# Kernel tuning notes

Measured on AMD Instinct MI355X. Metric: run time of the kernel, lower is better.

The kernel has to match this reference:

```python
import jax, jax.numpy as jnp
import numpy as np

B, N, D = 2, 2048, 2048
H, HKV, HD = 16, 4, 128  # n_heads, n_kv_heads, head_dim
G = H // HKV             # GQA group size


def setup_inputs() -> dict:
    key = jax.random.key(0)
    ks = jax.random.split(key, 5)
    x = jax.random.normal(ks[0], (B, N, D), jnp.float32)
    # rotary angles: standard 10000-base frequencies, half head_dim
    inv_freq = 1.0 / (10000.0 ** (jnp.arange(HD // 2, dtype=jnp.float32) / (HD // 2)))
    ang = jnp.arange(N, dtype=jnp.float32)[:, None] * inv_freq[None, :]  # [N, HD/2]
    cos = jnp.cos(ang)[None, :, None, :]  # [1, N, 1, HD/2]
    sin = jnp.sin(ang)[None, :, None, :]
    attn_mask = jnp.ones((B, N), jnp.float32)
    s = 0.02
    Wq = jax.random.normal(ks[1], (D, H * HD), jnp.float32) * s
    Wkv = jax.random.normal(ks[2], (D, 2 * HKV * HD), jnp.float32) * s
    Wo = jax.random.normal(ks[3], (H * HD, D), jnp.float32) * s
    bo = jnp.zeros((D,), jnp.float32)
    return {"x": x, "cos": cos, "sin": sin, "attn_mask": attn_mask,
            "Wq": Wq, "Wkv": Wkv, "Wo": Wo, "bo": bo}


def _rope(t, cos, sin):
    # t: [b, n, h, d]; rotate-half style split at d//2
    d2 = t.shape[-1] // 2
    t1, t2 = t[..., :d2], t[..., d2:]
    return jnp.concatenate([t1 * cos + t2 * sin, t2 * cos - t1 * sin], axis=-1)


def reference(x, cos, sin, attn_mask, Wq, Wkv, Wo, bo):
    b, n, _ = x.shape
    q = (x @ Wq).reshape(b, n, H, HD)
    kv = x @ Wkv
    k, v = jnp.split(kv, 2, axis=-1)
    k = k.reshape(b, n, HKV, HD)
    v = v.reshape(b, n, HKV, HD)
    q = _rope(q, cos, sin)
    k = _rope(k, cos, sin)
    # b n h d -> b h n d; group q heads: head H_idx maps to kv head H_idx % HKV
    # (einops '(r h)' repeat pattern => q reshaped as [b, G, HKV, n, d])
    q = q.transpose(0, 2, 1, 3).reshape(b, G, HKV, n, HD)
    k = k.transpose(0, 2, 1, 3)  # [b, HKV, n, d]
    v = v.transpose(0, 2, 1, 3)
    scale = HD ** -0.5
    attn = jnp.einsum('bghnd,bhmd->bghnm', q, k) * scale
    bias = (1.0 - attn_mask) * -1e9  # [b, n_keys]
    attn = attn + bias[:, None, None, None, :]
    attn = jax.nn.softmax(attn, axis=-1)
    out = jnp.einsum('bghnm,bhmd->bghnd', attn, v)
    # b (g h) n d -> b n (g h d)
    out = out.transpose(0, 3, 1, 2, 4).reshape(b, n, H * HD)
    return out @ Wo + bo
```

## Files before the change

### kernel.cpp

```cpp
#include <hip/hip_runtime.h>
#include <hip/hip_bf16.h>
#include <cstddef>

#define NB    2
#define NSEQ  2048
#define DMODEL 2048
#define NH    16
#define NKV   4
#define HDIM  128

typedef __attribute__((ext_vector_type(8))) short short8;
typedef __attribute__((ext_vector_type(4))) short short4v;
typedef __attribute__((ext_vector_type(4))) float floatx4;
typedef const __attribute__((address_space(1))) void* gptr_t;
typedef __attribute__((address_space(3))) void* lptr_t;

#if __has_builtin(__builtin_amdgcn_exp2f)
#define EXP2F(x) __builtin_amdgcn_exp2f(x)
#else
#define EXP2F(x) __expf((x) * 0.6931471805599453f)
#endif

__device__ inline unsigned short f2bf(float f) {
    unsigned int u = __float_as_uint(f);
    u += 0x7fffu + ((u >> 16) & 1u);
    return (unsigned short)(u >> 16);
}

__device__ inline unsigned int pk2bf_trunc(float a, float b) {
    return __builtin_amdgcn_perm(__float_as_uint(b), __float_as_uint(a), 0x07060302u);
}

__device__ inline floatx4 fzero4() {
    floatx4 v; v[0] = 0.f; v[1] = 0.f; v[2] = 0.f; v[3] = 0.f; return v;
}

__global__ void prep_k(const float* __restrict__ x, const float* __restrict__ Wq,
                       const float* __restrict__ Wkv, const float* __restrict__ Wo,
                       const float* __restrict__ mask,
                       unsigned short* __restrict__ xb,
                       unsigned short* __restrict__ W1T,
                       unsigned short* __restrict__ WoT,
                       float* __restrict__ bias2) {
    __shared__ float tile[32][33];
    const int bid = blockIdx.x, t = threadIdx.x;
    if (bid < 8192) {
        int i = bid * 256 + t;
        float4 v = ((const float4*)x)[i];
        ushort4 o;
        o.x = f2bf(v.x); o.y = f2bf(v.y); o.z = f2bf(v.z); o.w = f2bf(v.w);
        ((ushort4*)xb)[i] = o;
        return;
    }
    if (bid >= 18432) {
        int i = (bid - 18432) * 1024 + t * 4;
        float4 m = *(const float4*)(mask + i);
        const float c = -1.4426950408889634e9f;
        float4 o;
        o.x = (1.f - m.x) * c; o.y = (1.f - m.y) * c;
        o.z = (1.f - m.z) * c; o.w = (1.f - m.w) * c;
        *(float4*)(bias2 + i) = o;
        return;
    }
    const float* W; unsigned short* Wt; int N, local;
    if (bid < 12288)      { W = Wq;  Wt = W1T;                       N = 2048; local = bid - 8192; }
    else if (bid < 14336) { W = Wkv; Wt = W1T + (size_t)2048 * 2048; N = 1024; local = bid - 12288; }
    else                  { W = Wo;  Wt = WoT;                       N = 2048; local = bid - 14336; }
    const int K = 2048;
    int nt = N >> 5;
    int bx = local % nt, by = local / nt;
    int n0 = bx * 32, k0 = by * 32, tx = t & 31, ty = t >> 5;
#pragma unroll
    for (int i = 0; i < 4; i++)
        tile[ty + i * 8][tx] = W[(size_t)(k0 + ty + i * 8) * N + n0 + tx];
    __syncthreads();
#pragma unroll
    for (int i = 0; i < 4; i++)
        Wt[(size_t)(n0 + ty + i * 8) * K + k0 + tx] = f2bf(tile[tx][ty + i * 8]);
}

__global__ __launch_bounds__(256, 3) void gemm_bt(
    const unsigned short* __restrict__ A,
    const unsigned short* __restrict__ Bt,
    float* __restrict__ C,
    const float* __restrict__ bias,
    int M, int N, int K) {
    __shared__ __align__(16) unsigned short As[128 * 32];
    __shared__ __align__(16) unsigned short Bs[128 * 32];
    const int t = threadIdx.x;
    const int m0 = blockIdx.y * 128, n0 = blockIdx.x * 128;
    const int lane = t & 63, wave = t >> 6;
    const int ln = lane & 15, quad = lane >> 4;
    const int wm = (wave >> 1) * 64, wn = (wave & 1) * 64;
    floatx4 acc[4][4];
#pragma unroll
    for (int r = 0; r < 4; r++)
#pragma unroll
        for (int c = 0; c < 4; c++) acc[r][c] = fzero4();

    const int r0 = t >> 2, c0 = (t & 3) * 8;
    const int r1 = (t + 256) >> 2, c1 = ((t + 256) & 3) * 8;

    for (int kt = 0; kt < K; kt += 32) {
        const unsigned short* ga0 = A + (size_t)(m0 + r0) * K + kt + c0;
        const unsigned short* ga1 = A + (size_t)(m0 + r1) * K + kt + c1;
        const unsigned short* gb0 = Bt + (size_t)(n0 + r0) * K + kt + c0;
        const unsigned short* gb1 = Bt + (size_t)(n0 + r1) * K + kt + c1;
        __builtin_amdgcn_global_load_lds((gptr_t)ga0, (lptr_t)(As + t * 8), 16, 0, 0);
        __builtin_amdgcn_global_load_lds((gptr_t)ga1, (lptr_t)(As + (t + 256) * 8), 16, 0, 0);
        __builtin_amdgcn_global_load_lds((gptr_t)gb0, (lptr_t)(Bs + t * 8), 16, 0, 0);
        __builtin_amdgcn_global_load_lds((gptr_t)gb1, (lptr_t)(Bs + (t + 256) * 8), 16, 0, 0);
        __syncthreads();
        short8 af[4], bfr[4];
#pragma unroll
        for (int r = 0; r < 4; r++)
            af[r] = *(const short8*)(As + (wm + r * 16 + ln) * 32 + quad * 8);
#pragma unroll
        for (int c = 0; c < 4; c++)
            bfr[c] = *(const short8*)(Bs + (wn + c * 16 + ln) * 32 + quad * 8);
#pragma unroll
        for (int r = 0; r < 4; r++)
#pragma unroll
            for (int c = 0; c < 4; c++)
                acc[r][c] = __builtin_amdgcn_mfma_f32_16x16x32_bf16(af[r], bfr[c], acc[r][c], 0, 0, 0);
        __syncthreads();
    }
#pragma unroll
    for (int r = 0; r < 4; r++) {
        int mb = m0 + wm + r * 16 + quad * 4;
#pragma unroll
        for (int c = 0; c < 4; c++) {
            int col = n0 + wn + c * 16 + ln;
            float bv = bias ? bias[col] : 0.f;
#pragma unroll
            for (int g = 0; g < 4; g++)
                C[(size_t)(mb + g) * N + col] = acc[r][c][g] + bv;
        }
    }
}

__global__ __launch_bounds__(256, 3) void gemm_qkv_rope(
    const unsigned short* __restrict__ A,
    const unsigned short* __restrict__ Bt,
    const float* __restrict__ cosb,
    const float* __restrict__ sinb,
    unsigned short* __restrict__ Qb,
    unsigned short* __restrict__ Kb,
    unsigned short* __restrict__ Vt) {
    const int K = DMODEL;
    __shared__ __align__(16) unsigned short As[128 * 32];
    __shared__ __align__(16) unsigned short Bs[128 * 32];
    __shared__ __align__(16) unsigned short Vx[128 * 136];
    const int t = threadIdx.x;
    const int m0 = blockIdx.y * 128, n0 = blockIdx.x * 128;
    const int lane = t & 63, wave = t >> 6;
    const int ln = lane & 15, quad = lane >> 4;
    const int wm = (wave >> 1) * 64, bq = (wave & 1) * 32;
    floatx4 acc[4][4];
#pragma unroll
    for (int r = 0; r < 4; r++)
#pragma unroll
        for (int c = 0; c < 4; c++) acc[r][c] = fzero4();

    const int r0 = t >> 2, c0 = (t & 3) * 8;
    const int r1 = (t + 256) >> 2, c1 = ((t + 256) & 3) * 8;

    for (int kt = 0; kt < K; kt += 32) {
        const unsigned short* ga0 = A + (size_t)(m0 + r0) * K + kt + c0;
        const unsigned short* ga1 = A + (size_t)(m0 + r1) * K + kt + c1;
        const unsigned short* gb0 = Bt + (size_t)(n0 + r0) * K + kt + c0;
        const unsigned short* gb1 = Bt + (size_t)(n0 + r1) * K + kt + c1;
        __builtin_amdgcn_global_load_lds((gptr_t)ga0, (lptr_t)(As + t * 8), 16, 0, 0);
        __builtin_amdgcn_global_load_lds((gptr_t)ga1, (lptr_t)(As + (t + 256) * 8), 16, 0, 0);
        __builtin_amdgcn_global_load_lds((gptr_t)gb0, (lptr_t)(Bs + t * 8), 16, 0, 0);
        __builtin_amdgcn_global_load_lds((gptr_t)gb1, (lptr_t)(Bs + (t + 256) * 8), 16, 0, 0);
        __syncthreads();
        short8 af[4], bfr[4];
#pragma unroll
        for (int r = 0; r < 4; r++)
            af[r] = *(const short8*)(As + (wm + r * 16 + ln) * 32 + quad * 8);
#pragma unroll
        for (int c = 0; c < 4; c++)
            bfr[c] = *(const short8*)(
                Bs + (bq + (c & 1) * 16 + (c >> 1) * 64 + ln) * 32 + quad * 8);
#pragma unroll
        for (int r = 0; r < 4; r++)
#pragma unroll
            for (int c = 0; c < 4; c++)
                acc[r][c] = __builtin_amdgcn_mfma_f32_16x16x32_bf16(af[r], bfr[c], acc[r][c], 0, 0, 0);
        __syncthreads();
    }

    if (n0 < 2048) {
        const float qs = (float)(0.08838834764831845 * 1.4426950408889634);
        int h = n0 >> 7;
#pragma unroll
        for (int r = 0; r < 4; r++)
#pragma unroll
            for (int c = 0; c < 2; c++)
#pragma unroll
                for (int g = 0; g < 4; g++) {
                    int row = m0 + wm + r * 16 + quad * 4 + g;
                    int b = row >> 11, n = row & 2047;
                    int j = bq + c * 16 + ln;
                    float cv = cosb[n * 64 + j], sv = sinb[n * 64 + j];
                    float t1 = acc[r][c][g], t2 = acc[r][c + 2][g];
                    unsigned short* qp = Qb + ((size_t)(b * NH + h) * NSEQ + n) * 128;
                    qp[j]      = f2bf((t1 * cv + t2 * sv) * qs);
                    qp[j + 64] = f2bf((t2 * cv - t1 * sv) * qs);
                }
    } else if (n0 < 2560) {
        int hk = (n0 - 2048) >> 7;
#pragma unroll
        for (int r = 0; r < 4; r++)
#pragma unroll
            for (int c = 0; c < 2; c++)
#pragma unroll
                for (int g = 0; g < 4; g++) {
                    int row = m0 + wm + r * 16 + quad * 4 + g;
                    int b = row >> 11, n = row & 2047;
                    int j = bq + c * 16 + ln;
                    float cv = cosb[n * 64 + j], sv = sinb[n * 64 + j];
                    float t1 = acc[r][c][g], t2 = acc[r][c + 2][g];
                    unsigned short* kp = Kb + ((size_t)(b * NKV + hk) * NSEQ + n) * 128;
                    kp[j]      = f2bf(t1 * cv + t2 * sv);
                    kp[j + 64] = f2bf(t2 * cv - t1 * sv);
                }
    } else {
        int hk = (n0 - 2560) >> 7;
#pragma unroll
        for (int r = 0; r < 4; r++)
#pragma unroll
            for (int c = 0; c < 4; c++) {
                int d = bq + (c & 1) * 16 + (c >> 1) * 64 + ln;
                int s = wm + (r >> 1) * 32 + quad * 8 + (r & 1) * 4;
#pragma unroll
                for (int g = 0; g < 4; g++)
                    Vx[d * 136 + s + g] = f2bf(acc[r][c][g]);
            }
        __syncthreads();
        int b = m0 >> 11, nloc = m0 & 2047;
#pragma unroll
        for (int pass = 0; pass < 2; pass++) {
            int d = pass * 64 + (t >> 2), q4 = t & 3;
            unsigned short* vp =
                Vt + ((size_t)(b * NKV + hk) * 128 + d) * NSEQ + nloc + q4 * 32;
#pragma unroll
            for (int i = 0; i < 4; i++)
                *(short8*)(vp + i * 8) = *(const short8*)(Vx + d * 136 + q4 * 32 + i * 8);
        }
    }
}

__global__ __launch_bounds__(128, 2) void attn_k(
    const unsigned short* __restrict__ Qb,
    const unsigned short* __restrict__ Kb,
    const unsigned short* __restrict__ Vt,
    const float* __restrict__ bias2,
    unsigned short* __restrict__ Ab) {
    __shared__ __align__(16) unsigned short Ks[2 * 32 * 128];
    __shared__ __align__(16) unsigned short Vs[2 * 128 * 32];
    const int t = threadIdx.x, wave = t >> 6, lane = t & 63;
    const int ln = lane & 15, quad = lane >> 4;
    const int id = blockIdx.x;
    const int pair = id & 7, b = pair >> 2, kv = pair & 3;
    const int rest = id >> 3, g4 = rest & 3, h = g4 * 4 + kv, qb = rest >> 2;
    const int q0 = qb * 64;

    const unsigned short* Kbase = Kb + (size_t)(b * NKV + kv) * NSEQ * 128;
    const unsigned short* Vbase = Vt + (size_t)(b * NKV + kv) * 128 * NSEQ;
    const float* bbase = bias2 + b * NSEQ;

    const unsigned short* Qp =
        Qb + ((size_t)(b * NH + h) * NSEQ + q0 + wave * 32 + ln) * 128;
    short8 qf[2][4];
#pragma unroll
    for (int rt = 0; rt < 2; rt++)
#pragma unroll
        for (int kc = 0; kc < 4; kc++)
            qf[rt][kc] = *(const short8*)(Qp + rt * 16 * 128 + kc * 32 + quad * 8);

    const char* kp[4];
#pragma unroll
    for (int kc = 0; kc < 4; kc++)
        kp[kc] = (const char*)Ks + ln * 256 + (((kc * 4 + quad) ^ (ln & 7)) * 16);
    const char* vpp = (const char*)Vs + ln * 64 + ((quad ^ ((ln ^ (ln >> 2)) & 3)) * 16);

    floatx4 Oacc[2][8];
#pragma unroll
    for (int rt = 0; rt < 2; rt++)
#pragma unroll
        for (int d = 0; d < 8; d++) Oacc[rt][d] = fzero4();
    floatx4 Lacc[2];
    Lacc[0] = fzero4(); Lacc[1] = fzero4();

    short8 ones8;
#pragma unroll
    for (int i = 0; i < 8; i++) ones8[i] = (short)0x3F80;

    auto stage = [&](int ktn, int buf) {
#pragma unroll
        for (int i = 0; i < 4; i++) {
            int c = i * 128 + t, r = c >> 4, c8 = c & 15;
            __builtin_amdgcn_global_load_lds(
                (gptr_t)(Kbase + (size_t)(ktn + r) * 128 + ((c8 ^ (r & 7)) * 8)),
                (lptr_t)(Ks + buf * 4096 + c * 8), 16, 0, 0);
        }
#pragma unroll
        for (int i = 0; i < 4; i++) {
            int c = i * 128 + t, dr = c >> 2, c8 = c & 3;
            int f = (dr ^ (dr >> 2)) & 3;
            __builtin_amdgcn_global_load_lds(
                (gptr_t)(Vbase + (size_t)dr * NSEQ + ktn + ((c8 ^ f) * 8)),
                (lptr_t)(Vs + buf * 4096 + c * 8), 16, 0, 0);
        }
    };

    stage(0, 0);
    __syncthreads();

#pragma unroll 1
    for (int it2 = 0; it2 < NSEQ / 64; ++it2) {
#pragma unroll
        for (int half = 0; half < 2; ++half) {
            const int kt = (it2 * 2 + half) * 32;
            const int ktn = (kt + 32) & (NSEQ - 1);
            stage(ktn, half ^ 1);
            const int off = half * 8192;

            floatx4 biasv[2];
#pragma unroll
            for (int nj = 0; nj < 2; nj++)
                biasv[nj] = *(const floatx4*)(bbase + kt + nj * 16 + quad * 4);

            floatx4 sacc[2][2];
#pragma unroll
            for (int rt = 0; rt < 2; rt++)
#pragma unroll
                for (int nj = 0; nj < 2; nj++) sacc[rt][nj] = fzero4();
#pragma unroll
            for (int kc = 0; kc < 4; kc++) {
                short8 kfv[2];
#pragma unroll
                for (int nj = 0; nj < 2; nj++)
                    kfv[nj] = *(const short8*)(kp[kc] + off + nj * 4096);
#pragma unroll
                for (int rt = 0; rt < 2; rt++)
#pragma unroll
                    for (int nj = 0; nj < 2; nj++)
                        sacc[rt][nj] = __builtin_amdgcn_mfma_f32_16x16x32_bf16(
                            kfv[nj], qf[rt][kc], sacc[rt][nj], 0, 0, 0);
            }

            short8 pf[2];
#pragma unroll
            for (int rt = 0; rt < 2; rt++) {
                union { short8 s; unsigned int w[4]; } pu;
#pragma unroll
                for (int e = 0; e < 2; e++) {
                    float e0 = EXP2F(sacc[rt][e][0] + biasv[e][0]);
                    float e1 = EXP2F(sacc[rt][e][1] + biasv[e][1]);
                    float e2 = EXP2F(sacc[rt][e][2] + biasv[e][2]);
                    float e3 = EXP2F(sacc[rt][e][3] + biasv[e][3]);
                    pu.w[e * 2 + 0] = pk2bf_trunc(e0, e1);
                    pu.w[e * 2 + 1] = pk2bf_trunc(e2, e3);
                }
                pf[rt] = pu.s;
            }

#pragma unroll
            for (int rt = 0; rt < 2; rt++)
                Lacc[rt] = __builtin_amdgcn_mfma_f32_16x16x32_bf16(
                    ones8, pf[rt], Lacc[rt], 0, 0, 0);

#pragma unroll
            for (int dt = 0; dt < 8; dt++) {
                short8 vf = *(const short8*)(vpp + off + dt * 1024);
#pragma unroll
                for (int rt = 0; rt < 2; rt++)
                    Oacc[rt][dt] = __builtin_amdgcn_mfma_f32_16x16x32_bf16(
                        vf, pf[rt], Oacc[rt][dt], 0, 0, 0);
            }
            __syncthreads();
        }
    }

#pragma unroll
    for (int rt = 0; rt < 2; rt++) {
        float inv = 1.f / Lacc[rt][0];
        int row = q0 + wave * 32 + rt * 16 + ln;
        unsigned short* outp = Ab + (size_t)(b * NSEQ + row) * 2048 + h * 128;
#pragma unroll
        for (int dt = 0; dt < 8; dt++) {
            short4v o4;
#pragma unroll
            for (int g = 0; g < 4; g++) o4[g] = (short)f2bf(Oacc[rt][dt][g] * inv);
            *(short4v*)(outp + dt * 16 + quad * 4) = o4;
        }
    }
}

extern "C" void kernel_launch(void* const* d_in, const int* in_sizes, int n_in,
                              void* d_out, int out_size, void* d_ws, size_t ws_size,
                              hipStream_t stream) {
    const float* x    = (const float*)d_in[0];
    const float* cosb = (const float*)d_in[1];
    const float* sinb = (const float*)d_in[2];
    const float* mask = (const float*)d_in[3];
    const float* Wq   = (const float*)d_in[4];
    const float* Wkv  = (const float*)d_in[5];
    const float* Wo   = (const float*)d_in[6];
    const float* bo   = (const float*)d_in[7];
    float* out = (float*)d_out;

    char* ws = (char*)d_ws;
    unsigned short* xb  = (unsigned short*)ws; ws += (size_t)4096 * 2048 * 2;
    unsigned short* W1T = (unsigned short*)ws; ws += (size_t)3072 * 2048 * 2;
    unsigned short* WoT = (unsigned short*)ws; ws += (size_t)2048 * 2048 * 2;
    unsigned short* Qb  = (unsigned short*)ws; ws += (size_t)2 * 16 * 2048 * 128 * 2;
    unsigned short* Kb  = (unsigned short*)ws; ws += (size_t)2 * 4 * 2048 * 128 * 2;
    unsigned short* Vt  = (unsigned short*)ws; ws += (size_t)2 * 4 * 2048 * 128 * 2;
    unsigned short* Ab  = (unsigned short*)ws; ws += (size_t)2 * 2048 * 2048 * 2;
    float* bias2 = (float*)ws;                 ws += (size_t)NB * NSEQ * 4;

    prep_k<<<18436, 256, 0, stream>>>(x, Wq, Wkv, Wo, mask, xb, W1T, WoT, bias2);
    gemm_qkv_rope<<<dim3(24, 32), 256, 0, stream>>>(xb, W1T, cosb, sinb, Qb, Kb, Vt);
    attn_k<<<1024, 128, 0, stream>>>(Qb, Kb, Vt, bias2, Ab);
    gemm_bt<<<dim3(16, 32), 256, 0, stream>>>(Ab, WoT, out, bo, 4096, 2048, 2048);
}
```

Measured before the change: 310.0 us.

## Drop LDS staging in attention; load K/V fragments directly from global with register double-buffering

```diff
diff --git a/kernel.cpp b/kernel.cpp
--- a/kernel.cpp
+++ b/kernel.cpp
@@ -252,20 +252,18 @@
     }
 }
 
-__global__ __launch_bounds__(128, 2) void attn_k(
+__global__ __launch_bounds__(256, 2) void attn_k(
     const unsigned short* __restrict__ Qb,
     const unsigned short* __restrict__ Kb,
     const unsigned short* __restrict__ Vt,
     const float* __restrict__ bias2,
     unsigned short* __restrict__ Ab) {
-    __shared__ __align__(16) unsigned short Ks[2 * 32 * 128];
-    __shared__ __align__(16) unsigned short Vs[2 * 128 * 32];
     const int t = threadIdx.x, wave = t >> 6, lane = t & 63;
     const int ln = lane & 15, quad = lane >> 4;
     const int id = blockIdx.x;
     const int pair = id & 7, b = pair >> 2, kv = pair & 3;
     const int rest = id >> 3, g4 = rest & 3, h = g4 * 4 + kv, qb = rest >> 2;
-    const int q0 = qb * 64;
+    const int q0 = qb * 128;
 
     const unsigned short* Kbase = Kb + (size_t)(b * NKV + kv) * NSEQ * 128;
     const unsigned short* Vbase = Vt + (size_t)(b * NKV + kv) * 128 * NSEQ;
@@ -280,11 +278,8 @@
         for (int kc = 0; kc < 4; kc++)
             qf[rt][kc] = *(const short8*)(Qp + rt * 16 * 128 + kc * 32 + quad * 8);
 
-    const char* kp[4];
-#pragma unroll
-    for (int kc = 0; kc < 4; kc++)
-        kp[kc] = (const char*)Ks + ln * 256 + (((kc * 4 + quad) ^ (ln & 7)) * 16);
-    const char* vpp = (const char*)Vs + ln * 64 + ((quad ^ ((ln ^ (ln >> 2)) & 3)) * 16);
+    const unsigned short* kp0 = Kbase + ln * 128 + quad * 8;
+    const unsigned short* vp0 = Vbase + (size_t)ln * NSEQ + quad * 8;
 
     floatx4 Oacc[2][8];
 #pragma unroll
@@ -298,91 +293,77 @@
 #pragma unroll
     for (int i = 0; i < 8; i++) ones8[i] = (short)0x3F80;
 
-    auto stage = [&](int ktn, int buf) {
-#pragma unroll
-        for (int i = 0; i < 4; i++) {
-            int c = i * 128 + t, r = c >> 4, c8 = c & 15;
-            __builtin_amdgcn_global_load_lds(
-                (gptr_t)(Kbase + (size_t)(ktn + r) * 128 + ((c8 ^ (r & 7)) * 8)),
-                (lptr_t)(Ks + buf * 4096 + c * 8), 16, 0, 0);
+    short8 kfA[2][4], kfB[2][4];
+#pragma unroll
+    for (int nj = 0; nj < 2; nj++)
+#pragma unroll
+        for (int kc = 0; kc < 4; kc++)
+            kfA[nj][kc] = *(const short8*)(kp0 + nj * 16 * 128 + kc * 32);
+
+    auto phase = [&](short8 (&kcur)[2][4], short8 (&knxt)[2][4], int kt) {
+        short8 vf[8];
+#pragma unroll
+        for (int dt = 0; dt < 8; dt++)
+            vf[dt] = *(const short8*)(vp0 + (size_t)dt * 16 * NSEQ + kt);
+        const unsigned short* kn = kp0 + (size_t)(kt + 32) * 128;
+#pragma unroll
+        for (int nj = 0; nj < 2; nj++)
+#pragma unroll
+            for (int kc = 0; kc < 4; kc++)
+                knxt[nj][kc] = *(const short8*)(kn + nj * 16 * 128 + kc * 32);
+
+        floatx4 biasv[2];
+#pragma unroll
+        for (int nj = 0; nj < 2; nj++)
+            biasv[nj] = *(const floatx4*)(bbase + kt + nj * 16 + quad * 4);
+
+        floatx4 sacc[2][2];
+#pragma unroll
+        for (int rt = 0; rt < 2; rt++)
+#pragma unroll
+            for (int nj = 0; nj < 2; nj++) sacc[rt][nj] = fzero4();
+#pragma unroll
+        for (int kc = 0; kc < 4; kc++)
+#pragma unroll
+            for (int rt = 0; rt < 2; rt++)
+#pragma unroll
+                for (int nj = 0; nj < 2; nj++)
+                    sacc[rt][nj] = __builtin_amdgcn_mfma_f32_16x16x32_bf16(
+                        kcur[nj][kc], qf[rt][kc], sacc[rt][nj], 0, 0, 0);
+
+        short8 pf[2];
+#pragma unroll
+        for (int rt = 0; rt < 2; rt++) {
+            union { short8 s; unsigned int w[4]; } pu;
+#pragma unroll
+            for (int e = 0; e < 2; e++) {
+                float e0 = EXP2F(sacc[rt][e][0] + biasv[e][0]);
+                float e1 = EXP2F(sacc[rt][e][1] + biasv[e][1]);
+                float e2 = EXP2F(sacc[rt][e][2] + biasv[e][2]);
+                float e3 = EXP2F(sacc[rt][e][3] + biasv[e][3]);
+                pu.w[e * 2 + 0] = pk2bf_trunc(e0, e1);
+                pu.w[e * 2 + 1] = pk2bf_trunc(e2, e3);
+            }
+            pf[rt] = pu.s;
         }
-#pragma unroll
-        for (int i = 0; i < 4; i++) {
-            int c = i * 128 + t, dr = c >> 2, c8 = c & 3;
-            int f = (dr ^ (dr >> 2)) & 3;
-            __builtin_amdgcn_global_load_lds(
-                (gptr_t)(Vbase + (size_t)dr * NSEQ + ktn + ((c8 ^ f) * 8)),
-                (lptr_t)(Vs + buf * 4096 + c * 8), 16, 0, 0);
-        }
+
+#pragma unroll
+        for (int rt = 0; rt < 2; rt++)
+            Lacc[rt] = __builtin_amdgcn_mfma_f32_16x16x32_bf16(
+                ones8, pf[rt], Lacc[rt], 0, 0, 0);
+
+#pragma unroll
+        for (int dt = 0; dt < 8; dt++)
+#pragma unroll
+            for (int rt = 0; rt < 2; rt++)
+                Oacc[rt][dt] = __builtin_amdgcn_mfma_f32_16x16x32_bf16(
+                    vf[dt], pf[rt], Oacc[rt][dt], 0, 0, 0);
     };
 
-    stage(0, 0);
-    __syncthreads();
-
 #pragma unroll 1
-    for (int it2 = 0; it2 < NSEQ / 64; ++it2) {
-#pragma unroll
-        for (int half = 0; half < 2; ++half) {
-            const int kt = (it2 * 2 + half) * 32;
-            const int ktn = (kt + 32) & (NSEQ - 1);
-            stage(ktn, half ^ 1);
-            const int off = half * 8192;
-
-            floatx4 biasv[2];
-#pragma unroll
-            for (int nj = 0; nj < 2; nj++)
-                biasv[nj] = *(const floatx4*)(bbase + kt + nj * 16 + quad * 4);
-
-            floatx4 sacc[2][2];
-#pragma unroll
-            for (int rt = 0; rt < 2; rt++)
-#pragma unroll
-                for (int nj = 0; nj < 2; nj++) sacc[rt][nj] = fzero4();
-#pragma unroll
-            for (int kc = 0; kc < 4; kc++) {
-                short8 kfv[2];
-#pragma unroll
-                for (int nj = 0; nj < 2; nj++)
-                    kfv[nj] = *(const short8*)(kp[kc] + off + nj * 4096);
-#pragma unroll
-                for (int rt = 0; rt < 2; rt++)
-#pragma unroll
-                    for (int nj = 0; nj < 2; nj++)
-                        sacc[rt][nj] = __builtin_amdgcn_mfma_f32_16x16x32_bf16(
-                            kfv[nj], qf[rt][kc], sacc[rt][nj], 0, 0, 0);
-            }
-
-            short8 pf[2];
-#pragma unroll
-            for (int rt = 0; rt < 2; rt++) {
-                union { short8 s; unsigned int w[4]; } pu;
-#pragma unroll
-                for (int e = 0; e < 2; e++) {
-                    float e0 = EXP2F(sacc[rt][e][0] + biasv[e][0]);
-                    float e1 = EXP2F(sacc[rt][e][1] + biasv[e][1]);
-                    float e2 = EXP2F(sacc[rt][e][2] + biasv[e][2]);
-                    float e3 = EXP2F(sacc[rt][e][3] + biasv[e][3]);
-                    pu.w[e * 2 + 0] = pk2bf_trunc(e0, e1);
-                    pu.w[e * 2 + 1] = pk2bf_trunc(e2, e3);
-                }
-                pf[rt] = pu.s;
-            }
-
-#pragma unroll
-            for (int rt = 0; rt < 2; rt++)
-                Lacc[rt] = __builtin_amdgcn_mfma_f32_16x16x32_bf16(
-                    ones8, pf[rt], Lacc[rt], 0, 0, 0);
-
-#pragma unroll
-            for (int dt = 0; dt < 8; dt++) {
-                short8 vf = *(const short8*)(vpp + off + dt * 1024);
-#pragma unroll
-                for (int rt = 0; rt < 2; rt++)
-                    Oacc[rt][dt] = __builtin_amdgcn_mfma_f32_16x16x32_bf16(
-                        vf, pf[rt], Oacc[rt][dt], 0, 0, 0);
-            }
-            __syncthreads();
-        }
+    for (int it = 0; it < NSEQ / 32; it += 2) {
+        phase(kfA, kfB, it * 32);
+        phase(kfB, kfA, it * 32 + 32);
     }
 
 #pragma unroll
@@ -425,6 +406,6 @@
 
     prep_k<<<18436, 256, 0, stream>>>(x, Wq, Wkv, Wo, mask, xb, W1T, WoT, bias2);
     gemm_qkv_rope<<<dim3(24, 32), 256, 0, stream>>>(xb, W1T, cosb, sinb, Qb, Kb, Vt);
-    attn_k<<<1024, 128, 0, stream>>>(Qb, Kb, Vt, bias2, Ab);
+    attn_k<<<512, 256, 0, stream>>>(Qb, Kb, Vt, bias2, Ab);
     gemm_bt<<<dim3(16, 32), 256, 0, stream>>>(Ab, WoT, out, bo, 4096, 2048, 2048);
 }
```

Result: slower. 499.4 us (+61.1%).
